# Kernel tuning notes

Hardware: AMD Instinct MI355X
Metric: run time of the kernel (lower is better)

Reference implementation:

```python
import jax, jax.numpy as jnp
import numpy as np

N_NODES = 50000
N_EDGES = 500000
N_GRAPHS = 64
IN_DIM = 6
FFM_DIM = 128
GNN_DIM = 1024
OUT_DIM = 256
SCALES = (1.0, 5.0, 10.0, 30.0)
EPS = 1e-5


def setup_inputs() -> dict:
    key = jax.random.key(0)
    ks = jax.random.split(key, 16)
    x = jax.random.normal(ks[0], (N_NODES, IN_DIM), dtype=jnp.float32)
    edge_index = jax.random.randint(ks[1], (2, N_EDGES), 0, N_NODES, dtype=jnp.int32)
    node_coords = jax.random.normal(ks[2], (N_NODES, 3), dtype=jnp.float32)
    batch = jnp.sort(jax.random.randint(ks[3], (N_NODES,), 0, N_GRAPHS, dtype=jnp.int32))
    s6 = 1.0 / np.sqrt(IN_DIM)
    sg = 1.0 / np.sqrt(GNN_DIM)
    cat_dim = GNN_DIM + len(SCALES) * 2 * FFM_DIM
    sc = 1.0 / np.sqrt(cat_dim)
    return {
        "x": x, "edge_index": edge_index, "node_coords": node_coords, "batch": batch,
        "B": jax.random.normal(ks[4], (3, FFM_DIM), dtype=jnp.float32),
        "W1_l": jax.random.uniform(ks[5], (IN_DIM, GNN_DIM), jnp.float32, -s6, s6),
        "b1": jnp.zeros((GNN_DIM,), jnp.float32),
        "W1_r": jax.random.uniform(ks[6], (IN_DIM, GNN_DIM), jnp.float32, -s6, s6),
        "g1": jnp.ones((GNN_DIM,), jnp.float32), "be1": jnp.zeros((GNN_DIM,), jnp.float32),
        "W2_l": jax.random.uniform(ks[7], (GNN_DIM, GNN_DIM), jnp.float32, -sg, sg),
        "b2": jnp.zeros((GNN_DIM,), jnp.float32),
        "W2_r": jax.random.uniform(ks[8], (GNN_DIM, GNN_DIM), jnp.float32, -sg, sg),
        "g2": jnp.ones((GNN_DIM,), jnp.float32), "be2": jnp.zeros((GNN_DIM,), jnp.float32),
        "Wfc": jax.random.uniform(ks[9], (cat_dim, OUT_DIM), jnp.float32, -sc, sc),
        "bfc": jnp.zeros((OUT_DIM,), jnp.float32),
        "gfc": jnp.ones((OUT_DIM,), jnp.float32), "befc": jnp.zeros((OUT_DIM,), jnp.float32),
    }


def layer_norm(h, g, b):
    mu = jnp.mean(h, axis=-1, keepdims=True)
    var = jnp.mean(jnp.square(h - mu), axis=-1, keepdims=True)
    return (h - mu) * jax.lax.rsqrt(var + EPS) * g + b


def sage_conv(h, src, dst, Wl, bl, Wr):
    # mean aggregation of source features at destination nodes (PyG SAGEConv)
    agg = jax.ops.segment_sum(h[src], dst, num_segments=N_NODES)
    cnt = jax.ops.segment_sum(jnp.ones((src.shape[0],), h.dtype), dst, num_segments=N_NODES)
    agg = agg / jnp.maximum(cnt, 1.0)[:, None]
    return agg @ Wl + bl + h @ Wr


def reference(x, edge_index, node_coords, batch, B, W1_l, b1, W1_r, g1, be1,
              W2_l, b2, W2_r, g2, be2, Wfc, bfc, gfc, befc):
    src, dst = edge_index[0], edge_index[1]
    h = jax.nn.relu(layer_norm(sage_conv(x, src, dst, W1_l, b1, W1_r), g1, be1))
    h = jax.nn.relu(layer_norm(sage_conv(h, src, dst, W2_l, b2, W2_r), g2, be2))
    # multi-scale Fourier features on coordinates
    feats = []
    for s in SCALES:
        proj = (node_coords * s) @ B
        feats.append(jnp.sin(proj))
        feats.append(jnp.cos(proj))
    h_cat = jnp.concatenate([h] + feats, axis=1)
    # global mean pool per graph
    sums = jax.ops.segment_sum(h_cat, batch, num_segments=N_GRAPHS)
    cnts = jax.ops.segment_sum(jnp.ones((N_NODES,), h_cat.dtype), batch, num_segments=N_GRAPHS)
    h_g = sums / jnp.maximum(cnts, 1.0)[:, None]
    return layer_norm(h_g @ Wfc + bfc, gfc, befc)
```

## Files before the change

### kernel.cpp

```cpp
#include <hip/hip_runtime.h>
#include <hip/hip_bf16.h>


#define N_NODES 50000
#define N_EDGES 500000
#define N_GRAPHS 64
#define IN_DIM 6
#define GNN_DIM 1024
#define OUT_DIM 256
#define CAT_DIM 2048
#define M_PAD 50176

typedef __attribute__((ext_vector_type(8))) short short8;
typedef __attribute__((ext_vector_type(4))) float f32x4;

__device__ int g_cnt[N_NODES + 1];
__device__ int g_cursor[N_NODES];
__device__ int g_gcnt[N_GRAPHS];
__device__ int g_rowptr[N_NODES + 1];
__device__ int g_goff[N_GRAPHS + 1];
__device__ int g_esrc[N_EDGES];
__device__ __attribute__((aligned(256))) unsigned short g_w2lt[(size_t)GNN_DIM * GNN_DIM];
__device__ __attribute__((aligned(256))) unsigned short g_w2rt[(size_t)GNN_DIM * GNN_DIM];
__device__ float g_agg1[(size_t)N_NODES * IN_DIM];
__device__ __attribute__((aligned(256))) unsigned short g_h[(size_t)M_PAD * GNN_DIM];
__device__ __attribute__((aligned(256))) unsigned short g_agg2[(size_t)M_PAD * GNN_DIM];
__device__ __attribute__((aligned(256))) unsigned short g_h2[(size_t)M_PAD * GNN_DIM];
__device__ float g_lnsum[M_PAD];
__device__ float g_lnsq[M_PAD];
__device__ float g_gpool[(size_t)N_GRAPHS * CAT_DIM];

__device__ __forceinline__ float bflo(int u) { return __uint_as_float(((unsigned)u) << 16); }
__device__ __forceinline__ float bfhi(int u) { return __uint_as_float(((unsigned)u) & 0xffff0000u); }
__device__ __forceinline__ unsigned short f2bf(float f) {
    unsigned u = __float_as_uint(f);
    unsigned rounded = u + 0x7fff + ((u >> 16) & 1);
    return (unsigned short)(rounded >> 16);
}
__device__ __forceinline__ int pack2(unsigned short a, unsigned short b) {
    return (int)((unsigned)a | ((unsigned)b << 16));
}

__global__ void zero_kernel() {
    int i = blockIdx.x * 256 + threadIdx.x;
    if (i <= N_NODES) g_cnt[i] = 0;
    if (i < N_NODES) g_cursor[i] = 0;
    if (i < N_GRAPHS) g_gcnt[i] = 0;
    if (i < M_PAD) { g_lnsum[i] = 0.f; g_lnsq[i] = 0.f; }
    if (i < N_GRAPHS * CAT_DIM) g_gpool[i] = 0.f;
}

__global__ void count_kernel(const int* __restrict__ dst, const int* __restrict__ batch) {
    int i = blockIdx.x * 256 + threadIdx.x;
    if (i < N_EDGES) atomicAdd(&g_cnt[dst[i]], 1);
    if (i < N_NODES) atomicAdd(&g_gcnt[batch[i]], 1);
}

__global__ __launch_bounds__(1024) void scan_kernel() {
    const int CH = 49;
    int t = threadIdx.x;
    int base = t * CH;
    int s = 0;
    #pragma unroll
    for (int i = 0; i < CH; ++i) {
        int n = base + i;
        s += (n < N_NODES) ? g_cnt[n] : 0;
    }
    int lane = t & 63, w = t >> 6;
    int x = s;
    #pragma unroll
    for (int off = 1; off < 64; off <<= 1) {
        int y = __shfl_up(x, off);
        if (lane >= off) x += y;
    }
    __shared__ int wsum[16], woff[16];
    if (lane == 63) wsum[w] = x;
    __syncthreads();
    if (t == 0) { int a = 0; for (int i = 0; i < 16; ++i) { woff[i] = a; a += wsum[i]; } }
    __syncthreads();
    int excl = x - s + woff[w];
    #pragma unroll
    for (int i = 0; i < CH; ++i) {
        int n = base + i;
        if (n <= N_NODES) g_rowptr[n] = excl;
        if (n < N_NODES) excl += g_cnt[n];
    }
}

__global__ void goff_kernel() {
    if (threadIdx.x == 0 && blockIdx.x == 0) {
        int acc = 0;
        for (int g = 0; g < N_GRAPHS; ++g) { g_goff[g] = acc; acc += g_gcnt[g]; }
        g_goff[N_GRAPHS] = acc;
    }
}

__global__ void scatter_kernel(const int* __restrict__ src, const int* __restrict__ dst) {
    int e = blockIdx.x * 256 + threadIdx.x;
    if (e >= N_EDGES) return;
    int d = dst[e];
    int pos = atomicAdd(&g_cursor[d], 1);
    g_esrc[g_rowptr[d] + pos] = src[e];
}

__global__ void transpose_bf16(const float* __restrict__ W, unsigned short* __restrict__ Wt) {
    __shared__ float tile[32][33];
    int bx = blockIdx.x & 31, by = blockIdx.x >> 5;
    int tx = threadIdx.x & 31, ty = threadIdx.x >> 5;
    for (int i = 0; i < 32; i += 8)
        tile[ty + i][tx] = W[(size_t)(by * 32 + ty + i) * GNN_DIM + bx * 32 + tx];
    __syncthreads();
    for (int i = 0; i < 32; i += 8)
        Wt[(size_t)(bx * 32 + ty + i) * GNN_DIM + by * 32 + tx] = f2bf(tile[tx][ty + i]);
}

__global__ void l1_agg_kernel(const float* __restrict__ x) {
    int id = blockIdx.x * 256 + threadIdx.x;
    int n = id >> 3, slot = id & 7;
    if (n >= N_NODES || slot >= IN_DIM) return;
    int beg = g_rowptr[n], end = g_rowptr[n + 1];
    float s = 0.f;
    for (int i = beg; i < end; ++i) s += x[(size_t)g_esrc[i] * IN_DIM + slot];
    g_agg1[n * IN_DIM + slot] = s / (float)max(end - beg, 1);
}

__global__ __launch_bounds__(256) void l1_transform_kernel(
        const float* __restrict__ x,
        const float* __restrict__ W1l, const float* __restrict__ b1,
        const float* __restrict__ W1r, const float* __restrict__ g1,
        const float* __restrict__ be1) {
    int t = threadIdx.x;
    int nb = blockIdx.x * 8;
    float4 wl[6], wr[6];
    #pragma unroll
    for (int k = 0; k < 6; ++k) {
        wl[k] = *(const float4*)&W1l[k * GNN_DIM + t * 4];
        wr[k] = *(const float4*)&W1r[k * GNN_DIM + t * 4];
    }
    float4 bb = *(const float4*)&b1[t * 4];
    float4 gg = *(const float4*)&g1[t * 4];
    float4 be = *(const float4*)&be1[t * 4];
    __shared__ float sx[48], sa[48];
    if (t < 48) sx[t] = x[nb * 6 + t];
    else if (t < 96) sa[t - 48] = g_agg1[nb * 6 + (t - 48)];
    __syncthreads();
    __shared__ float s1[4], s2[4];
    for (int u = 0; u < 8; ++u) {
        int n = nb + u;
        float4 v = bb;
        #pragma unroll
        for (int k = 0; k < 6; ++k) {
            float a = sa[u * 6 + k], xx = sx[u * 6 + k];
            v.x += a * wl[k].x + xx * wr[k].x;
            v.y += a * wl[k].y + xx * wr[k].y;
            v.z += a * wl[k].z + xx * wr[k].z;
            v.w += a * wl[k].w + xx * wr[k].w;
        }
        float sum = v.x + v.y + v.z + v.w;
        float sq  = v.x*v.x + v.y*v.y + v.z*v.z + v.w*v.w;
        #pragma unroll
        for (int off = 32; off; off >>= 1) { sum += __shfl_xor(sum, off); sq += __shfl_xor(sq, off); }
        if ((t & 63) == 0) { s1[t >> 6] = sum; s2[t >> 6] = sq; }
        __syncthreads();
        sum = s1[0] + s1[1] + s1[2] + s1[3];
        sq  = s2[0] + s2[1] + s2[2] + s2[3];
        __syncthreads();
        float mu = sum * (1.f / GNN_DIM);
        float var = sq * (1.f / GNN_DIM) - mu * mu;
        float rstd = rsqrtf(var + 1e-5f);
        float y0 = fmaxf((v.x - mu) * rstd * gg.x + be.x, 0.f);
        float y1 = fmaxf((v.y - mu) * rstd * gg.y + be.y, 0.f);
        float y2 = fmaxf((v.z - mu) * rstd * gg.z + be.z, 0.f);
        float y3 = fmaxf((v.w - mu) * rstd * gg.w + be.w, 0.f);
        int2 pk;
        pk.x = pack2(f2bf(y0), f2bf(y1));
        pk.y = pack2(f2bf(y2), f2bf(y3));
        *(int2*)(g_h + (size_t)n * GNN_DIM + t * 4) = pk;
    }
}

__global__ __launch_bounds__(256) void l2_agg_kernel() {
    int w = threadIdx.x >> 6, lane = threadIdx.x & 63;
    int n = blockIdx.x * 2 + (w >> 1);
    int hw = w & 1;
    int beg = g_rowptr[n], end = g_rowptr[n + 1];
    float s[8];
    #pragma unroll
    for (int j = 0; j < 8; ++j) s[j] = 0.f;
    const int4* hp = (const int4*)g_h;
    int off = hw * 64 + lane;
    for (int i = beg; i < end; i += 8) {
        int idx[8]; float msk[8]; int4 v[8];
        #pragma unroll
        for (int j = 0; j < 8; ++j) {
            int e = i + j;
            int cl = (e < end) ? e : beg;
            idx[j] = g_esrc[cl];
            msk[j] = (e < end) ? 1.f : 0.f;
        }
        #pragma unroll
        for (int j = 0; j < 8; ++j) v[j] = hp[(size_t)idx[j] * 128 + off];
        #pragma unroll
        for (int j = 0; j < 8; ++j) {
            float m = msk[j];
            s[0] += m * bflo(v[j].x); s[1] += m * bfhi(v[j].x);
            s[2] += m * bflo(v[j].y); s[3] += m * bfhi(v[j].y);
            s[4] += m * bflo(v[j].z); s[5] += m * bfhi(v[j].z);
            s[6] += m * bflo(v[j].w); s[7] += m * bfhi(v[j].w);
        }
    }
    float inv = 1.f / (float)max(end - beg, 1);
    int4 o;
    o.x = pack2(f2bf(s[0] * inv), f2bf(s[1] * inv));
    o.y = pack2(f2bf(s[2] * inv), f2bf(s[3] * inv));
    o.z = pack2(f2bf(s[4] * inv), f2bf(s[5] * inv));
    o.w = pack2(f2bf(s[6] * inv), f2bf(s[7] * inv));
    *(int4*)(g_agg2 + (size_t)n * GNN_DIM + (size_t)off * 8) = o;
}

#define BM 128
#define BN 128
#define BK 64

__global__ __launch_bounds__(256) void gemm2_kernel(const float* __restrict__ bias) {
    __shared__ __attribute__((aligned(16))) unsigned short As[BM * BK];
    __shared__ __attribute__((aligned(16))) unsigned short Bs[BN * BK];
    int i = blockIdx.x;
    int xcd = i & 7;
    int j = i >> 3;
    int bm = xcd * 49 + (j >> 3);
    int bn = j & 7;
    int row0 = bm * BM, col0 = bn * BN;
    int t = threadIdx.x;
    int lane = t & 63, wid = t >> 6;
    int wr = wid >> 1, wc = wid & 1;
    f32x4 acc[4][4] = {};
    int c0 = t;
    for (int seg = 0; seg < 2; ++seg) {
        const unsigned short* A  = seg ? g_h : g_agg2;
        const unsigned short* Bt = seg ? g_w2rt : g_w2lt;
        for (int k0 = 0; k0 < GNN_DIM; k0 += BK) {
            __syncthreads();
            #pragma unroll
            for (int u = 0; u < 4; ++u) {
                int c = c0 + u * 256;
                int r = c >> 3;
                int kb = (c & 7) * 16;
                int kbs = kb ^ ((r & 7) << 4);
                __builtin_amdgcn_global_load_lds(
                    (const __attribute__((address_space(1))) void*)(A + (size_t)(row0 + r) * GNN_DIM + k0 + (kbs >> 1)),
                    (__attribute__((address_space(3))) void*)(As + c * 8), 16, 0, 0);
            }
            #pragma unroll
            for (int u = 0; u < 4; ++u) {
                int c = c0 + u * 256;
                int r = c >> 3;
                int kb = (c & 7) * 16;
                int kbs = kb ^ ((r & 7) << 4);
                __builtin_amdgcn_global_load_lds(
                    (const __attribute__((address_space(1))) void*)(Bt + (size_t)(col0 + r) * GNN_DIM + k0 + (kbs >> 1)),
                    (__attribute__((address_space(3))) void*)(Bs + c * 8), 16, 0, 0);
            }
            asm volatile("s_waitcnt vmcnt(0)" ::: "memory");
            __syncthreads();
            #pragma unroll
            for (int kk = 0; kk < BK; kk += 32) {
                short8 a[4], b[4];
                int krd = kk + (lane >> 4) * 8;
                #pragma unroll
                for (int m = 0; m < 4; ++m) {
                    int row = wr * 64 + m * 16 + (lane & 15);
                    int ks = ((krd * 2) ^ ((row & 7) << 4)) >> 1;
                    a[m] = *(const short8*)&As[row * BK + ks];
                }
                #pragma unroll
                for (int n = 0; n < 4; ++n) {
                    int row = wc * 64 + n * 16 + (lane & 15);
                    int ks = ((krd * 2) ^ ((row & 7) << 4)) >> 1;
                    b[n] = *(const short8*)&Bs[row * BK + ks];
                }
                #pragma unroll
                for (int m = 0; m < 4; ++m)
                    #pragma unroll
                    for (int n = 0; n < 4; ++n)
                        acc[m][n] = __builtin_amdgcn_mfma_f32_16x16x32_bf16(a[m], b[n], acc[m][n], 0, 0, 0);
            }
        }
    }
    #pragma unroll
    for (int m = 0; m < 4; ++m) {
        float rs[4] = {0.f, 0.f, 0.f, 0.f}, rq[4] = {0.f, 0.f, 0.f, 0.f};
        int rbase = row0 + wr * 64 + m * 16 + (lane >> 4) * 4;
        #pragma unroll
        for (int n = 0; n < 4; ++n) {
            int col = col0 + wc * 64 + n * 16 + (lane & 15);
            float bv = bias[col];
            #pragma unroll
            for (int r = 0; r < 4; ++r) {
                float v = acc[m][n][r] + bv;
                g_h2[(size_t)(rbase + r) * GNN_DIM + col] = f2bf(v);
                rs[r] += v; rq[r] += v * v;
            }
        }
        #pragma unroll
        for (int r = 0; r < 4; ++r) {
            float a = rs[r], b = rq[r];
            #pragma unroll
            for (int mk = 1; mk < 16; mk <<= 1) { a += __shfl_xor(a, mk); b += __shfl_xor(b, mk); }
            if ((lane & 15) == 0) {
                atomicAdd(&g_lnsum[rbase + r], a);
                atomicAdd(&g_lnsq[rbase + r], b);
            }
        }
    }
}

__global__ __launch_bounds__(256) void pool_h_kernel(const float* __restrict__ g2,
                                                     const float* __restrict__ be2) {
    int g = blockIdx.x >> 3, sl = blockIdx.x & 7;
    int t = threadIdx.x;
    int beg = g_goff[g], end = g_goff[g + 1];
    int cnt = end - beg;
    int per = (cnt + 7) >> 3;
    int s0 = beg + sl * per, s1 = min(s0 + per, end);
    if (s0 >= s1) return;
    float4 gg = *(const float4*)&g2[t * 4];
    float4 be = *(const float4*)&be2[t * 4];
    float a0 = 0.f, a1 = 0.f, a2 = 0.f, a3 = 0.f;
    for (int n = s0; n < s1; ++n) {
        float mu = g_lnsum[n] * (1.f / GNN_DIM);
        float var = g_lnsq[n] * (1.f / GNN_DIM) - mu * mu;
        float rstd = rsqrtf(var + 1e-5f);
        int2 w = *(const int2*)(g_h2 + (size_t)n * GNN_DIM + t * 4);
        a0 += fmaxf((bflo(w.x) - mu) * rstd * gg.x + be.x, 0.f);
        a1 += fmaxf((bfhi(w.x) - mu) * rstd * gg.y + be.y, 0.f);
        a2 += fmaxf((bflo(w.y) - mu) * rstd * gg.z + be.z, 0.f);
        a3 += fmaxf((bfhi(w.y) - mu) * rstd * gg.w + be.w, 0.f);
    }
    atomicAdd(&g_gpool[g * CAT_DIM + t * 4 + 0], a0);
    atomicAdd(&g_gpool[g * CAT_DIM + t * 4 + 1], a1);
    atomicAdd(&g_gpool[g * CAT_DIM + t * 4 + 2], a2);
    atomicAdd(&g_gpool[g * CAT_DIM + t * 4 + 3], a3);
}

__global__ __launch_bounds__(256) void pool_f_kernel(const float* __restrict__ coords,
                                                     const float* __restrict__ Bmat) {
    int g = blockIdx.x >> 1, sl = blockIdx.x & 1;
    int t = threadIdx.x;
    int beg = g_goff[g], end = g_goff[g + 1];
    int cnt = end - beg;
    int per = (cnt + 1) >> 1;
    int s0 = beg + sl * per, s1 = min(s0 + per, end);
    const float SC[4] = {1.f, 5.f, 10.f, 30.f};
    int si0 = t >> 7, c0 = t & 127;
    int si1 = si0 + 2;
    float b00 = Bmat[c0] * SC[si0], b01 = Bmat[128 + c0] * SC[si0], b02 = Bmat[256 + c0] * SC[si0];
    float b10 = Bmat[c0] * SC[si1], b11 = Bmat[128 + c0] * SC[si1], b12 = Bmat[256 + c0] * SC[si1];
    float ss0 = 0.f, cs0 = 0.f, ss1 = 0.f, cs1 = 0.f;
    __shared__ float sc[256 * 3];
    for (int base = s0; base < s1; base += 256) {
        int m = min(256, s1 - base);
        __syncthreads();
        for (int q = t; q < 3 * m; q += 256) sc[q] = coords[base * 3 + q];
        __syncthreads();
        for (int i = 0; i < m; ++i) {
            float x0 = sc[i * 3], y0 = sc[i * 3 + 1], z0 = sc[i * 3 + 2];
            float p0 = x0 * b00 + y0 * b01 + z0 * b02;
            float p1 = x0 * b10 + y0 * b11 + z0 * b12;
            ss0 += __sinf(p0); cs0 += __cosf(p0);
            ss1 += __sinf(p1); cs1 += __cosf(p1);
        }
    }
    if (s0 < s1) {
        float* gp = g_gpool + g * CAT_DIM + GNN_DIM;
        atomicAdd(&gp[si0 * 256 + c0], ss0);
        atomicAdd(&gp[si0 * 256 + 128 + c0], cs0);
        atomicAdd(&gp[si1 * 256 + c0], ss1);
        atomicAdd(&gp[si1 * 256 + 128 + c0], cs1);
    }
}

__global__ __launch_bounds__(256) void final_kernel(
        const float* __restrict__ Wfc, const float* __restrict__ bfc,
        const float* __restrict__ gfc, const float* __restrict__ befc,
        float* __restrict__ out) {
    int g = blockIdx.x, t = threadIdx.x;
    int beg = g_goff[g], end = g_goff[g + 1];
    float inv = 1.f / (float)max(end - beg, 1);
    __shared__ float hg[CAT_DIM];
    for (int i = t; i < CAT_DIM; i += 256) hg[i] = g_gpool[g * CAT_DIM + i] * inv;
    __syncthreads();
    float acc = bfc[t];
    for (int k = 0; k < CAT_DIM; ++k) acc = fmaf(hg[k], Wfc[(size_t)k * OUT_DIM + t], acc);
    float sum = acc, sq = acc * acc;
    #pragma unroll
    for (int off = 32; off; off >>= 1) { sum += __shfl_xor(sum, off); sq += __shfl_xor(sq, off); }
    __shared__ float s1[4], s2[4];
    if ((t & 63) == 0) { s1[t >> 6] = sum; s2[t >> 6] = sq; }
    __syncthreads();
    sum = s1[0] + s1[1] + s1[2] + s1[3];
    sq  = s2[0] + s2[1] + s2[2] + s2[3];
    float mu = sum * (1.f / OUT_DIM);
    float var = sq * (1.f / OUT_DIM) - mu * mu;
    float rstd = rsqrtf(var + 1e-5f);
    out[g * OUT_DIM + t] = (acc - mu) * rstd * gfc[t] + befc[t];
}

extern "C" void kernel_launch(void* const* d_in, const int* in_sizes, int n_in,
                              void* d_out, int out_size, void* d_ws, size_t ws_size,
                              hipStream_t stream) {
    const float* x      = (const float*)d_in[0];
    const int*   ei     = (const int*)d_in[1];
    const float* coords = (const float*)d_in[2];
    const int*   batch  = (const int*)d_in[3];
    const float* Bmat   = (const float*)d_in[4];
    const float* W1l    = (const float*)d_in[5];
    const float* b1     = (const float*)d_in[6];
    const float* W1r    = (const float*)d_in[7];
    const float* g1     = (const float*)d_in[8];
    const float* be1    = (const float*)d_in[9];
    const float* W2l    = (const float*)d_in[10];
    const float* b2     = (const float*)d_in[11];
    const float* W2r    = (const float*)d_in[12];
    const float* g2     = (const float*)d_in[13];
    const float* be2    = (const float*)d_in[14];
    const float* Wfc    = (const float*)d_in[15];
    const float* bfc    = (const float*)d_in[16];
    const float* gfc    = (const float*)d_in[17];
    const float* befc   = (const float*)d_in[18];
    const int* src = ei;
    const int* dst = ei + N_EDGES;
    float* out = (float*)d_out;
    (void)in_sizes; (void)n_in; (void)out_size; (void)d_ws; (void)ws_size;

    unsigned short* w2lt;  hipGetSymbolAddress((void**)&w2lt, HIP_SYMBOL(g_w2lt));
    unsigned short* w2rt;  hipGetSymbolAddress((void**)&w2rt, HIP_SYMBOL(g_w2rt));

    zero_kernel<<<512, 256, 0, stream>>>();
    count_kernel<<<(N_EDGES + 255) / 256, 256, 0, stream>>>(dst, batch);
    scan_kernel<<<1, 1024, 0, stream>>>();
    goff_kernel<<<1, 64, 0, stream>>>();
    scatter_kernel<<<(N_EDGES + 255) / 256, 256, 0, stream>>>(src, dst);

    transpose_bf16<<<1024, 256, 0, stream>>>(W2l, w2lt);
    transpose_bf16<<<1024, 256, 0, stream>>>(W2r, w2rt);

    l1_agg_kernel<<<(N_NODES * 8 + 255) / 256, 256, 0, stream>>>(x);
    l1_transform_kernel<<<N_NODES / 8, 256, 0, stream>>>(x, W1l, b1, W1r, g1, be1);

    l2_agg_kernel<<<N_NODES / 2, 256, 0, stream>>>();

    gemm2_kernel<<<(M_PAD / BM) * (GNN_DIM / BN), 256, 0, stream>>>(b2);

    pool_h_kernel<<<N_GRAPHS * 8, 256, 0, stream>>>(g2, be2);
    pool_f_kernel<<<N_GRAPHS * 2, 256, 0, stream>>>(coords, Bmat);

    final_kernel<<<N_GRAPHS, 256, 0, stream>>>(Wfc, bfc, gfc, befc, out);
}
```

Before: 907.0 us.

## Move LN2 stats into pooling, merge transposes, widen l2 agg per wave

```diff
diff --git a/kernel.cpp b/kernel.cpp
--- a/kernel.cpp
+++ b/kernel.cpp
@@ -26,8 +26,6 @@
 __device__ __attribute__((aligned(256))) unsigned short g_h[(size_t)M_PAD * GNN_DIM];
 __device__ __attribute__((aligned(256))) unsigned short g_agg2[(size_t)M_PAD * GNN_DIM];
 __device__ __attribute__((aligned(256))) unsigned short g_h2[(size_t)M_PAD * GNN_DIM];
-__device__ float g_lnsum[M_PAD];
-__device__ float g_lnsq[M_PAD];
 __device__ float g_gpool[(size_t)N_GRAPHS * CAT_DIM];
 
 __device__ __forceinline__ float bflo(int u) { return __uint_as_float(((unsigned)u) << 16); }
@@ -46,7 +44,6 @@
     if (i <= N_NODES) g_cnt[i] = 0;
     if (i < N_NODES) g_cursor[i] = 0;
     if (i < N_GRAPHS) g_gcnt[i] = 0;
-    if (i < M_PAD) { g_lnsum[i] = 0.f; g_lnsq[i] = 0.f; }
     if (i < N_GRAPHS * CAT_DIM) g_gpool[i] = 0.f;
 }
 
@@ -103,9 +100,13 @@
     g_esrc[g_rowptr[d] + pos] = src[e];
 }
 
-__global__ void transpose_bf16(const float* __restrict__ W, unsigned short* __restrict__ Wt) {
+__global__ void transpose_bf16(const float* __restrict__ WA, const float* __restrict__ WB,
+                               unsigned short* __restrict__ TA, unsigned short* __restrict__ TB) {
     __shared__ float tile[32][33];
-    int bx = blockIdx.x & 31, by = blockIdx.x >> 5;
+    int id = blockIdx.x & 1023;
+    const float* W = (blockIdx.x >> 10) ? WB : WA;
+    unsigned short* Wt = (blockIdx.x >> 10) ? TB : TA;
+    int bx = id & 31, by = id >> 5;
     int tx = threadIdx.x & 31, ty = threadIdx.x >> 5;
     for (int i = 0; i < 32; i += 8)
         tile[ty + i][tx] = W[(size_t)(by * 32 + ty + i) * GNN_DIM + bx * 32 + tx];
@@ -181,16 +182,14 @@
 
 __global__ __launch_bounds__(256) void l2_agg_kernel() {
     int w = threadIdx.x >> 6, lane = threadIdx.x & 63;
-    int n = blockIdx.x * 2 + (w >> 1);
-    int hw = w & 1;
+    int n = blockIdx.x * 4 + w;
     int beg = g_rowptr[n], end = g_rowptr[n + 1];
-    float s[8];
-    #pragma unroll
-    for (int j = 0; j < 8; ++j) s[j] = 0.f;
+    float s[16];
+    #pragma unroll
+    for (int j = 0; j < 16; ++j) s[j] = 0.f;
     const int4* hp = (const int4*)g_h;
-    int off = hw * 64 + lane;
     for (int i = beg; i < end; i += 8) {
-        int idx[8]; float msk[8]; int4 v[8];
+        int idx[8]; float msk[8]; int4 va[8], vb[8];
         #pragma unroll
         for (int j = 0; j < 8; ++j) {
             int e = i + j;
@@ -199,23 +198,35 @@
             msk[j] = (e < end) ? 1.f : 0.f;
         }
         #pragma unroll
-        for (int j = 0; j < 8; ++j) v[j] = hp[(size_t)idx[j] * 128 + off];
+        for (int j = 0; j < 8; ++j) {
+            va[j] = hp[(size_t)idx[j] * 128 + lane];
+            vb[j] = hp[(size_t)idx[j] * 128 + 64 + lane];
+        }
         #pragma unroll
         for (int j = 0; j < 8; ++j) {
             float m = msk[j];
-            s[0] += m * bflo(v[j].x); s[1] += m * bfhi(v[j].x);
-            s[2] += m * bflo(v[j].y); s[3] += m * bfhi(v[j].y);
-            s[4] += m * bflo(v[j].z); s[5] += m * bfhi(v[j].z);
-            s[6] += m * bflo(v[j].w); s[7] += m * bfhi(v[j].w);
+            s[0]  += m * bflo(va[j].x); s[1]  += m * bfhi(va[j].x);
+            s[2]  += m * bflo(va[j].y); s[3]  += m * bfhi(va[j].y);
+            s[4]  += m * bflo(va[j].z); s[5]  += m * bfhi(va[j].z);
+            s[6]  += m * bflo(va[j].w); s[7]  += m * bfhi(va[j].w);
+            s[8]  += m * bflo(vb[j].x); s[9]  += m * bfhi(vb[j].x);
+            s[10] += m * bflo(vb[j].y); s[11] += m * bfhi(vb[j].y);
+            s[12] += m * bflo(vb[j].z); s[13] += m * bfhi(vb[j].z);
+            s[14] += m * bflo(vb[j].w); s[15] += m * bfhi(vb[j].w);
         }
     }
     float inv = 1.f / (float)max(end - beg, 1);
-    int4 o;
-    o.x = pack2(f2bf(s[0] * inv), f2bf(s[1] * inv));
-    o.y = pack2(f2bf(s[2] * inv), f2bf(s[3] * inv));
-    o.z = pack2(f2bf(s[4] * inv), f2bf(s[5] * inv));
-    o.w = pack2(f2bf(s[6] * inv), f2bf(s[7] * inv));
-    *(int4*)(g_agg2 + (size_t)n * GNN_DIM + (size_t)off * 8) = o;
+    int4 o0, o1;
+    o0.x = pack2(f2bf(s[0] * inv),  f2bf(s[1] * inv));
+    o0.y = pack2(f2bf(s[2] * inv),  f2bf(s[3] * inv));
+    o0.z = pack2(f2bf(s[4] * inv),  f2bf(s[5] * inv));
+    o0.w = pack2(f2bf(s[6] * inv),  f2bf(s[7] * inv));
+    o1.x = pack2(f2bf(s[8] * inv),  f2bf(s[9] * inv));
+    o1.y = pack2(f2bf(s[10] * inv), f2bf(s[11] * inv));
+    o1.z = pack2(f2bf(s[12] * inv), f2bf(s[13] * inv));
+    o1.w = pack2(f2bf(s[14] * inv), f2bf(s[15] * inv));
+    *(int4*)(g_agg2 + (size_t)n * GNN_DIM + (size_t)lane * 8) = o0;
+    *(int4*)(g_agg2 + (size_t)n * GNN_DIM + 512 + (size_t)lane * 8) = o1;
 }
 
 #define BM 128
@@ -289,27 +300,15 @@
     }
     #pragma unroll
     for (int m = 0; m < 4; ++m) {
-        float rs[4] = {0.f, 0.f, 0.f, 0.f}, rq[4] = {0.f, 0.f, 0.f, 0.f};
-        int rbase = row0 + wr * 64 + m * 16 + (lane >> 4) * 4;
         #pragma unroll
         for (int n = 0; n < 4; ++n) {
             int col = col0 + wc * 64 + n * 16 + (lane & 15);
+            int rbase = row0 + wr * 64 + m * 16 + (lane >> 4) * 4;
             float bv = bias[col];
             #pragma unroll
             for (int r = 0; r < 4; ++r) {
                 float v = acc[m][n][r] + bv;
                 g_h2[(size_t)(rbase + r) * GNN_DIM + col] = f2bf(v);
-                rs[r] += v; rq[r] += v * v;
-            }
-        }
-        #pragma unroll
-        for (int r = 0; r < 4; ++r) {
-            float a = rs[r], b = rq[r];
-            #pragma unroll
-            for (int mk = 1; mk < 16; mk <<= 1) { a += __shfl_xor(a, mk); b += __shfl_xor(b, mk); }
-            if ((lane & 15) == 0) {
-                atomicAdd(&g_lnsum[rbase + r], a);
-                atomicAdd(&g_lnsq[rbase + r], b);
             }
         }
     }
@@ -322,20 +321,33 @@
     int beg = g_goff[g], end = g_goff[g + 1];
     int cnt = end - beg;
     int per = (cnt + 7) >> 3;
-    int s0 = beg + sl * per, s1 = min(s0 + per, end);
-    if (s0 >= s1) return;
+    int s0 = beg + sl * per, s1v = min(s0 + per, end);
+    if (s0 >= s1v) return;
     float4 gg = *(const float4*)&g2[t * 4];
     float4 be = *(const float4*)&be2[t * 4];
+    __shared__ float r1[4], r2[4];
     float a0 = 0.f, a1 = 0.f, a2 = 0.f, a3 = 0.f;
-    for (int n = s0; n < s1; ++n) {
-        float mu = g_lnsum[n] * (1.f / GNN_DIM);
-        float var = g_lnsq[n] * (1.f / GNN_DIM) - mu * mu;
+    int2 wv = *(const int2*)(g_h2 + (size_t)s0 * GNN_DIM + t * 4);
+    for (int n = s0; n < s1v; ++n) {
+        int2 w = wv;
+        if (n + 1 < s1v) wv = *(const int2*)(g_h2 + (size_t)(n + 1) * GNN_DIM + t * 4);
+        float v0 = bflo(w.x), v1 = bfhi(w.x), v2 = bflo(w.y), v3 = bfhi(w.y);
+        float sum = v0 + v1 + v2 + v3;
+        float sq  = v0*v0 + v1*v1 + v2*v2 + v3*v3;
+        #pragma unroll
+        for (int off = 32; off; off >>= 1) { sum += __shfl_xor(sum, off); sq += __shfl_xor(sq, off); }
+        if ((t & 63) == 0) { r1[t >> 6] = sum; r2[t >> 6] = sq; }
+        __syncthreads();
+        sum = r1[0] + r1[1] + r1[2] + r1[3];
+        sq  = r2[0] + r2[1] + r2[2] + r2[3];
+        __syncthreads();
+        float mu = sum * (1.f / GNN_DIM);
+        float var = sq * (1.f / GNN_DIM) - mu * mu;
         float rstd = rsqrtf(var + 1e-5f);
-        int2 w = *(const int2*)(g_h2 + (size_t)n * GNN_DIM + t * 4);
-        a0 += fmaxf((bflo(w.x) - mu) * rstd * gg.x + be.x, 0.f);
-        a1 += fmaxf((bfhi(w.x) - mu) * rstd * gg.y + be.y, 0.f);
-        a2 += fmaxf((bflo(w.y) - mu) * rstd * gg.z + be.z, 0.f);
-        a3 += fmaxf((bfhi(w.y) - mu) * rstd * gg.w + be.w, 0.f);
+        a0 += fmaxf((v0 - mu) * rstd * gg.x + be.x, 0.f);
+        a1 += fmaxf((v1 - mu) * rstd * gg.y + be.y, 0.f);
+        a2 += fmaxf((v2 - mu) * rstd * gg.z + be.z, 0.f);
+        a3 += fmaxf((v3 - mu) * rstd * gg.w + be.w, 0.f);
     }
     atomicAdd(&g_gpool[g * CAT_DIM + t * 4 + 0], a0);
     atomicAdd(&g_gpool[g * CAT_DIM + t * 4 + 1], a1);
@@ -442,13 +454,12 @@
     goff_kernel<<<1, 64, 0, stream>>>();
     scatter_kernel<<<(N_EDGES + 255) / 256, 256, 0, stream>>>(src, dst);
 
-    transpose_bf16<<<1024, 256, 0, stream>>>(W2l, w2lt);
-    transpose_bf16<<<1024, 256, 0, stream>>>(W2r, w2rt);
+    transpose_bf16<<<2048, 256, 0, stream>>>(W2l, W2r, w2lt, w2rt);
 
     l1_agg_kernel<<<(N_NODES * 8 + 255) / 256, 256, 0, stream>>>(x);
     l1_transform_kernel<<<N_NODES / 8, 256, 0, stream>>>(x, W1l, b1, W1r, g1, be1);
 
-    l2_agg_kernel<<<N_NODES / 2, 256, 0, stream>>>();
+    l2_agg_kernel<<<N_NODES / 4, 256, 0, stream>>>();
 
     gemm2_kernel<<<(M_PAD / BM) * (GNN_DIM / BN), 256, 0, stream>>>(b2);
 
```

Measured after the change: 895.5 us. No clear change (-1.3%).
